# Kernel optimization log

Measured on AMD Instinct MI355X. Metric: run time of the kernel, lower is better.

## Reference

```python
import jax, jax.numpy as jnp
import numpy as np

NEG_SLOPE = 0.2  # PyG GATConv default negative_slope


def gat_conv(x, src, dst, n_nodes, W, a_src, a_dst, b, concat):
    # x: [N, F_in], W: [F_in, H*C], a_src/a_dst: [H, C], b: [H*C] or [C]
    H, C = a_src.shape
    h = (x @ W).reshape(n_nodes, H, C)              # [N, H, C]
    e_s = jnp.sum(h * a_src, axis=-1)               # [N, H]
    e_d = jnp.sum(h * a_dst, axis=-1)               # [N, H]
    e = jax.nn.leaky_relu(e_s[src] + e_d[dst], NEG_SLOPE)  # [E, H]
    # segment softmax over incoming edges of each destination node
    m = jax.ops.segment_max(e, dst, num_segments=n_nodes)
    m = jnp.where(jnp.isfinite(m), m, 0.0)
    p = jnp.exp(e - m[dst])                         # [E, H]
    s = jax.ops.segment_sum(p, dst, num_segments=n_nodes)
    alpha = p / (s[dst] + 1e-16)                    # [E, H]
    out = jax.ops.segment_sum(h[src] * alpha[:, :, None], dst, num_segments=n_nodes)  # [N, H, C]
    out = out.reshape(n_nodes, H * C) if concat else out.mean(axis=1)
    return out + b


def setup_inputs() -> dict:
    key = jax.random.key(0)
    ks = jax.random.split(key, 20)
    N, E = 50000, 800000
    F_in, C, H = 128, 64, 4
    sc = 0.05
    inp = {
        "x": jax.random.normal(ks[0], (N, F_in), dtype=jnp.float32),
        "edge_index": jax.random.randint(ks[1], (2, E), 0, N, dtype=jnp.int64),
        # conv1: F_in -> C x H heads, concat
        "W1": jax.random.normal(ks[2], (F_in, H * C), dtype=jnp.float32) * sc,
        "a1_src": jax.random.normal(ks[3], (H, C), dtype=jnp.float32) * sc,
        "a1_dst": jax.random.normal(ks[4], (H, C), dtype=jnp.float32) * sc,
        "b1": jnp.zeros((H * C,), dtype=jnp.float32),
        # conv2: H*C -> C x H heads, concat
        "W2": jax.random.normal(ks[5], (H * C, H * C), dtype=jnp.float32) * sc,
        "a2_src": jax.random.normal(ks[6], (H, C), dtype=jnp.float32) * sc,
        "a2_dst": jax.random.normal(ks[7], (H, C), dtype=jnp.float32) * sc,
        "b2": jnp.zeros((H * C,), dtype=jnp.float32),
        # conv3: H*C -> C, 1 head, concat=False (mean)
        "W3": jax.random.normal(ks[8], (H * C, C), dtype=jnp.float32) * sc,
        "a3_src": jax.random.normal(ks[9], (1, C), dtype=jnp.float32) * sc,
        "a3_dst": jax.random.normal(ks[10], (1, C), dtype=jnp.float32) * sc,
        "b3": jnp.zeros((C,), dtype=jnp.float32),
        # node classification head: C -> 2
        "cls_W": jax.random.normal(ks[11], (C, 2), dtype=jnp.float32) * sc,
        "cls_b": jnp.zeros((2,), dtype=jnp.float32),
    }
    return inp


def reference(x, edge_index, W1, a1_src, a1_dst, b1, W2, a2_src, a2_dst, b2,
              W3, a3_src, a3_dst, b3, cls_W, cls_b):
    N = x.shape[0]
    # PyG GATConv default: add self loops
    loop = jnp.arange(N, dtype=edge_index.dtype)
    ei = jnp.concatenate([edge_index, jnp.stack([loop, loop])], axis=1)
    src, dst = ei[0], ei[1]

    h = jax.nn.elu(gat_conv(x, src, dst, N, W1, a1_src, a1_dst, b1, concat=True))
    h = jax.nn.elu(gat_conv(h, src, dst, N, W2, a2_src, a2_dst, b2, concat=True))
    h = gat_conv(h, src, dst, N, W3, a3_src, a3_dst, b3, concat=False)  # [N, C]

    node_output = h @ cls_W + cls_b  # [N, 2]
    link_embedding = h               # [N, C]
    return node_output, link_embedding
```

## Files before the change

kernel.cpp:

```cpp
#include <hip/hip_runtime.h>
#include <math.h>


typedef unsigned short ushort;
typedef __attribute__((ext_vector_type(8))) short bf16x8;
typedef __attribute__((ext_vector_type(4))) float f32x4;

static __device__ __forceinline__ ushort f2bf(float f) {
    unsigned x = __float_as_uint(f);
    unsigned r = (x + 0x7FFF + ((x >> 16) & 1)) >> 16;
    return (ushort)r;
}
static __device__ __forceinline__ float bf2f(ushort u) {
    return __uint_as_float(((unsigned)u) << 16);
}


__global__ void count_deg(const int* __restrict__ ei, int E, int* __restrict__ deg) {
    int i = blockIdx.x * blockDim.x + threadIdx.x;
    int stride = gridDim.x * blockDim.x;
    for (int e = i; e < E; e += stride) {
        int d = ei[E + e];
        atomicAdd(&deg[d], 1);
    }
}

__global__ void scan_local(const int* __restrict__ deg, int* __restrict__ offsets,
                           int* __restrict__ blockSums, int N) {
    int tid = threadIdx.x;
    int lane = tid & 63;
    int wv = tid >> 6;
    int base = blockIdx.x * 1024 + tid * 4;
    int v[4];
#pragma unroll
    for (int j = 0; j < 4; ++j) {
        int idx = base + j;
        v[j] = (idx < N) ? (deg[idx] + 1) : 0;
    }
    int tsum = v[0] + v[1] + v[2] + v[3];
    int inc = tsum;
#pragma unroll
    for (int off = 1; off < 64; off <<= 1) {
        int u = __shfl_up(inc, off);
        if (lane >= off) inc += u;
    }
    __shared__ int wtot[4];
    if (lane == 63) wtot[wv] = inc;
    __syncthreads();
    int wbase = 0;
#pragma unroll
    for (int w = 0; w < 4; ++w)
        if (w < wv) wbase += wtot[w];
    int run = wbase + inc - tsum;
#pragma unroll
    for (int j = 0; j < 4; ++j) {
        int idx = base + j;
        if (idx < N) offsets[idx] = run;
        run += v[j];
    }
    if (tid == 255) blockSums[blockIdx.x] = wbase + inc;
}

__global__ void scan_blocks(const int* __restrict__ blockSums, int* __restrict__ blockBase,
                            int* __restrict__ offsets, int N, int nblk) {
    int lane = threadIdx.x & 63;
    int v = (lane < nblk) ? blockSums[lane] : 0;
    int inc = v;
#pragma unroll
    for (int off = 1; off < 64; off <<= 1) {
        int u = __shfl_up(inc, off);
        if (lane >= off) inc += u;
    }
    if (lane < nblk) blockBase[lane] = inc - v;
    if (lane == 63) offsets[N] = inc;
}

__global__ void scan_add(int* __restrict__ offsets, const int* __restrict__ blockBase, int N) {
    int i = blockIdx.x * blockDim.x + threadIdx.x;
    if (i < N) offsets[i] += blockBase[i >> 10];
}

__global__ void fill_self(const int* __restrict__ offsets, int* __restrict__ counter,
                          int* __restrict__ csr_src, int N) {
    int i = blockIdx.x * blockDim.x + threadIdx.x;
    if (i < N) {
        csr_src[offsets[i]] = i;
        counter[i] = 1;
    }
}

__global__ void fill_edges(const int* __restrict__ ei, int E,
                           const int* __restrict__ offsets, int* __restrict__ counter,
                           int* __restrict__ csr_src) {
    int i = blockIdx.x * blockDim.x + threadIdx.x;
    int stride = gridDim.x * blockDim.x;
    for (int e = i; e < E; e += stride) {
        int s = ei[e];
        int d = ei[E + e];
        int pos = offsets[d] + atomicAdd(&counter[d], 1);
        csr_src[pos] = s;
    }
}


__global__ void xsplit(const float* __restrict__ X, ushort* __restrict__ Xh,
                       ushort* __restrict__ Xl, int total4) {
    int i = blockIdx.x * blockDim.x + threadIdx.x;
    if (i >= total4) return;
    float4 v = *(const float4*)(X + (size_t)i * 4);
    ushort4 h, l;
    h.x = f2bf(v.x); l.x = f2bf(v.x - bf2f(h.x));
    h.y = f2bf(v.y); l.y = f2bf(v.y - bf2f(h.y));
    h.z = f2bf(v.z); l.z = f2bf(v.z - bf2f(h.z));
    h.w = f2bf(v.w); l.w = f2bf(v.w - bf2f(h.w));
    *(ushort4*)(Xh + (size_t)i * 4) = h;
    *(ushort4*)(Xl + (size_t)i * 4) = l;
}

__global__ void wsplit_t(const float* __restrict__ W, ushort* __restrict__ Wth,
                         ushort* __restrict__ Wtl, int K, int N) {
    int id = blockIdx.x * blockDim.x + threadIdx.x;
    if (id >= K * N) return;
    int k = id % K, n = id / K;
    float v = W[(size_t)k * N + n];
    ushort h = f2bf(v);
    Wth[id] = h;
    Wtl[id] = f2bf(v - bf2f(h));
}


template<int BN>
__global__ __launch_bounds__(256) void gemm_mfma(const ushort* __restrict__ Ah,
                                                 const ushort* __restrict__ Al,
                                                 const ushort* __restrict__ Bh,
                                                 const ushort* __restrict__ Bl,
                                                 float* __restrict__ Cmat,
                                                 int M, int N, int K) {
    constexpr int BK = 32, PAD = 8;
    constexpr int WAVES_N = BN / 64;
    constexpr int WAVES_M = 4 / WAVES_N;
    constexpr int WTM = 128 / WAVES_M;
    constexpr int MI = WTM / 16;
    constexpr int NI = 4;
    __shared__ ushort Atile[128][BK + PAD];
    __shared__ ushort Btile[BN][BK + PAD];

    int tid = threadIdx.x;
    int lane = tid & 63;
    int wid = tid >> 6;
    int fr = lane & 15;
    int fg = lane >> 4;
    int wm0 = (wid / WAVES_N) * WTM;
    int wn0 = (wid % WAVES_N) * 64;
    int mBase = blockIdx.x * 128;
    int nBase = blockIdx.y * BN;

    f32x4 acc[MI][NI];
#pragma unroll
    for (int mi = 0; mi < MI; ++mi)
#pragma unroll
        for (int ni = 0; ni < NI; ++ni) acc[mi][ni] = (f32x4)0.0f;

    const int KI = K / BK;
    for (int seg = 0; seg < 3; ++seg) {
        const ushort* Ap = (seg == 1) ? Al : Ah;
        const ushort* Bp = (seg == 2) ? Bl : Bh;
        for (int t = 0; t < KI; ++t) {
            int k0 = t * BK;
#pragma unroll
            for (int i = 0; i < 2; ++i) {
                int u = tid + i * 256;
                int row = u >> 2;
                int sl = (u & 3) * 8;
                int gm = mBase + row;
                if (gm >= M) gm = M - 1;
                bf16x8 v = *(const bf16x8*)(Ap + (size_t)gm * K + k0 + sl);
                *(bf16x8*)&Atile[row][sl] = v;
            }
#pragma unroll
            for (int i = 0; i < BN * BK / 8 / 256; ++i) {
                int u = tid + i * 256;
                int row = u >> 2;
                int sl = (u & 3) * 8;
                int gn = nBase + row;
                bf16x8 v = *(const bf16x8*)(Bp + (size_t)gn * K + k0 + sl);
                *(bf16x8*)&Btile[row][sl] = v;
            }
            __syncthreads();
            bf16x8 af[MI], bfr[NI];
#pragma unroll
            for (int mi = 0; mi < MI; ++mi)
                af[mi] = *(const bf16x8*)&Atile[wm0 + mi * 16 + fr][fg * 8];
#pragma unroll
            for (int ni = 0; ni < NI; ++ni)
                bfr[ni] = *(const bf16x8*)&Btile[wn0 + ni * 16 + fr][fg * 8];
#pragma unroll
            for (int mi = 0; mi < MI; ++mi)
#pragma unroll
                for (int ni = 0; ni < NI; ++ni)
                    acc[mi][ni] = __builtin_amdgcn_mfma_f32_16x16x32_bf16(
                        af[mi], bfr[ni], acc[mi][ni], 0, 0, 0);
            __syncthreads();
        }
    }

#pragma unroll
    for (int mi = 0; mi < MI; ++mi) {
#pragma unroll
        for (int j = 0; j < 4; ++j) {
            int gm = mBase + wm0 + mi * 16 + fg * 4 + j;
            if (gm >= M) continue;
#pragma unroll
            for (int ni = 0; ni < NI; ++ni) {
                int gn = nBase + wn0 + ni * 16 + fr;
                Cmat[(size_t)gm * N + gn] = acc[mi][ni][j];
            }
        }
    }
}


template<int HC, int H>
__global__ void attn_coef(const float* __restrict__ h,
                          const float* __restrict__ a_src,
                          const float* __restrict__ a_dst,
                          float* __restrict__ e_s, float* __restrict__ e_d,
                          ushort* __restrict__ hb, int N) {
    int wid = (int)((blockIdx.x * (size_t)blockDim.x + threadIdx.x) >> 6);
    int lane = threadIdx.x & 63;
    if (wid >= N) return;
    if constexpr (HC == 256) {
        float4 hv = *(const float4*)(h + (size_t)wid * 256 + lane * 4);
        float4 as = *(const float4*)(a_src + lane * 4);
        float4 ad = *(const float4*)(a_dst + lane * 4);
        ushort4 q;
        q.x = f2bf(hv.x); q.y = f2bf(hv.y); q.z = f2bf(hv.z); q.w = f2bf(hv.w);
        *(ushort4*)(hb + (size_t)wid * 256 + lane * 4) = q;
        float ps = hv.x * as.x + hv.y * as.y + hv.z * as.z + hv.w * as.w;
        float pd = hv.x * ad.x + hv.y * ad.y + hv.z * ad.z + hv.w * ad.w;
#pragma unroll
        for (int off = 1; off <= 8; off <<= 1) {
            ps += __shfl_xor(ps, off);
            pd += __shfl_xor(pd, off);
        }
        if ((lane & 15) == 0) {
            int hd = lane >> 4;
            e_s[(size_t)wid * H + hd] = ps;
            e_d[(size_t)wid * H + hd] = pd;
        }
    } else {
        float hv = h[(size_t)wid * HC + lane];
        hb[(size_t)wid * HC + lane] = f2bf(hv);
        float ps = hv * a_src[lane];
        float pd = hv * a_dst[lane];
#pragma unroll
        for (int off = 1; off <= 32; off <<= 1) {
            ps += __shfl_xor(ps, off);
            pd += __shfl_xor(pd, off);
        }
        if (lane == 0) {
            e_s[wid] = ps;
            e_d[wid] = pd;
        }
    }
}


template<int HC, int H, bool ELU, int U, bool SPLIT>
__global__ void aggregate(const ushort* __restrict__ hb,
                          const float* __restrict__ e_s, const float* __restrict__ e_d,
                          const int* __restrict__ offsets, const int* __restrict__ csr_src,
                          const float* __restrict__ bias,
                          float* __restrict__ out,
                          ushort* __restrict__ oh, ushort* __restrict__ ol, int N) {
    int wid = (int)((blockIdx.x * (size_t)blockDim.x + threadIdx.x) >> 6);
    int lane = threadIdx.x & 63;
    if (wid >= N) return;
    constexpr int VEC = HC / 64;
    constexpr int C = HC / H;
    int hd = (lane * VEC) / C;
    float ed = e_d[(size_t)wid * H + hd];
    int beg = offsets[wid], end = offsets[wid + 1];
    float m = -1e30f, s = 0.0f;
    float acc[VEC];
#pragma unroll
    for (int j = 0; j < VEC; ++j) acc[j] = 0.0f;

    for (int k = beg; k < end; k += U) {
        int sidx[U];
#pragma unroll
        for (int u = 0; u < U; ++u) {
            int kk = k + u;
            kk = (kk < end) ? kk : end - 1;
            sidx[u] = csr_src[kk];
        }
        float e[U];
#pragma unroll
        for (int u = 0; u < U; ++u) e[u] = e_s[(size_t)sidx[u] * H + hd];
        ushort4 hv4[U];
        ushort  hv1[U];
        if constexpr (VEC == 4) {
#pragma unroll
            for (int u = 0; u < U; ++u)
                hv4[u] = *(const ushort4*)(hb + (size_t)sidx[u] * HC + lane * 4);
        } else {
#pragma unroll
            for (int u = 0; u < U; ++u)
                hv1[u] = hb[(size_t)sidx[u] * HC + lane];
        }
#pragma unroll
        for (int u = 0; u < U; ++u) {
            float t = e[u] + ed;
            t = (t >= 0.0f) ? t : 0.2f * t;
            e[u] = (k + u < end) ? t : -1e30f;
        }
        float bm = -1e30f;
#pragma unroll
        for (int u = 0; u < U; ++u) bm = fmaxf(bm, e[u]);
        float nm = fmaxf(m, bm);
        float r = __expf(m - nm);
        float p[U];
        float psum = 0.0f;
#pragma unroll
        for (int u = 0; u < U; ++u) { p[u] = __expf(e[u] - nm); psum += p[u]; }
        s = s * r + psum;
        if constexpr (VEC == 4) {
#pragma unroll
            for (int j = 0; j < 4; ++j) acc[j] *= r;
#pragma unroll
            for (int u = 0; u < U; ++u) {
                acc[0] += p[u] * bf2f(hv4[u].x);
                acc[1] += p[u] * bf2f(hv4[u].y);
                acc[2] += p[u] * bf2f(hv4[u].z);
                acc[3] += p[u] * bf2f(hv4[u].w);
            }
        } else {
            acc[0] *= r;
#pragma unroll
            for (int u = 0; u < U; ++u) acc[0] += p[u] * bf2f(hv1[u]);
        }
        m = nm;
    }
    float inv = 1.0f / (s + 1e-16f);
    float o[VEC];
#pragma unroll
    for (int j = 0; j < VEC; ++j) {
        int f = lane * VEC + j;
        o[j] = acc[j] * inv + bias[f];
        if constexpr (ELU) o[j] = (o[j] > 0.0f) ? o[j] : expm1f(o[j]);
    }
    if constexpr (SPLIT) {
        if constexpr (VEC == 4) {
            ushort4 h4, l4;
            h4.x = f2bf(o[0]); l4.x = f2bf(o[0] - bf2f(h4.x));
            h4.y = f2bf(o[1]); l4.y = f2bf(o[1] - bf2f(h4.y));
            h4.z = f2bf(o[2]); l4.z = f2bf(o[2] - bf2f(h4.z));
            h4.w = f2bf(o[3]); l4.w = f2bf(o[3] - bf2f(h4.w));
            *(ushort4*)(oh + (size_t)wid * HC + lane * 4) = h4;
            *(ushort4*)(ol + (size_t)wid * HC + lane * 4) = l4;
        } else {
            ushort h1 = f2bf(o[0]);
            oh[(size_t)wid * HC + lane] = h1;
            ol[(size_t)wid * HC + lane] = f2bf(o[0] - bf2f(h1));
        }
    } else {
#pragma unroll
        for (int j = 0; j < VEC; ++j)
            out[(size_t)wid * HC + lane * VEC + j] = o[j];
    }
}


__global__ void cls_head(const float* __restrict__ h3, const float* __restrict__ W,
                         const float* __restrict__ b, float* __restrict__ out, int N) {
    int wid = (int)((blockIdx.x * (size_t)blockDim.x + threadIdx.x) >> 6);
    int lane = threadIdx.x & 63;
    if (wid >= N) return;
    float v = h3[(size_t)wid * 64 + lane];
    float p0 = v * W[lane * 2 + 0];
    float p1 = v * W[lane * 2 + 1];
#pragma unroll
    for (int off = 1; off <= 32; off <<= 1) {
        p0 += __shfl_xor(p0, off);
        p1 += __shfl_xor(p1, off);
    }
    if (lane == 0) {
        out[(size_t)wid * 2 + 0] = p0 + b[0];
        out[(size_t)wid * 2 + 1] = p1 + b[1];
    }
}


extern "C" void kernel_launch(void* const* d_in, const int* in_sizes, int n_in,
                              void* d_out, int out_size, void* d_ws, size_t ws_size,
                              hipStream_t stream) {
    const float* x      = (const float*)d_in[0];
    const int*   ei     = (const int*)d_in[1];
    const float* W1     = (const float*)d_in[2];
    const float* a1_src = (const float*)d_in[3];
    const float* a1_dst = (const float*)d_in[4];
    const float* b1     = (const float*)d_in[5];
    const float* W2     = (const float*)d_in[6];
    const float* a2_src = (const float*)d_in[7];
    const float* a2_dst = (const float*)d_in[8];
    const float* b2     = (const float*)d_in[9];
    const float* W3     = (const float*)d_in[10];
    const float* a3_src = (const float*)d_in[11];
    const float* a3_dst = (const float*)d_in[12];
    const float* b3     = (const float*)d_in[13];
    const float* cls_W  = (const float*)d_in[14];
    const float* cls_b  = (const float*)d_in[15];

    const int N = in_sizes[0] / 128;
    const int E = in_sizes[1] / 2;
    const int ET = E + N;
    const int HC = 256;
    const int nScanBlk = (N + 1023) / 1024;

    char* w = (char*)d_ws;
    auto carve = [&](size_t bytes) {
        char* p = w;
        w += (bytes + 255) & ~(size_t)255;
        return p;
    };
    int*    deg     = (int*)   carve((size_t)N * 4);
    int*    counter = (int*)   carve((size_t)N * 4);
    int*    offsets = (int*)   carve((size_t)(N + 1) * 4);
    int*    csr_src = (int*)   carve((size_t)ET * 4);
    int*    blkSums = (int*)   carve((size_t)64 * 4);
    int*    blkBase = (int*)   carve((size_t)64 * 4);
    float*  e_s     = (float*) carve((size_t)N * 4 * 4);
    float*  e_d     = (float*) carve((size_t)N * 4 * 4);
    float*  hbuf    = (float*) carve((size_t)N * HC * 4);
    ushort* hb      = (ushort*)carve((size_t)N * HC * 2);
    ushort* Ahi     = (ushort*)carve((size_t)N * HC * 2);
    ushort* Alo     = (ushort*)carve((size_t)N * HC * 2);
    ushort* W1th    = (ushort*)carve((size_t)128 * 256 * 2);
    ushort* W1tl    = (ushort*)carve((size_t)128 * 256 * 2);
    ushort* W2th    = (ushort*)carve((size_t)256 * 256 * 2);
    ushort* W2tl    = (ushort*)carve((size_t)256 * 256 * 2);
    ushort* W3th    = (ushort*)carve((size_t)256 * 64 * 2);
    ushort* W3tl    = (ushort*)carve((size_t)256 * 64 * 2);
    (void)ws_size;

    float* out_node = (float*)d_out;
    float* out_link = (float*)d_out + 2 * (size_t)N;

    hipMemsetAsync(deg, 0, (size_t)N * 4, stream);
    int eblocks = (E + 255) / 256;
    if (eblocks > 2048) eblocks = 2048;
    count_deg<<<eblocks, 256, 0, stream>>>(ei, E, deg);
    scan_local<<<nScanBlk, 256, 0, stream>>>(deg, offsets, blkSums, N);
    scan_blocks<<<1, 64, 0, stream>>>(blkSums, blkBase, offsets, N, nScanBlk);
    scan_add<<<(N + 255) / 256, 256, 0, stream>>>(offsets, blkBase, N);
    fill_self<<<(N + 255) / 256, 256, 0, stream>>>(offsets, counter, csr_src, N);
    fill_edges<<<eblocks, 256, 0, stream>>>(ei, E, offsets, counter, csr_src);

    xsplit<<<(N * 128 / 4 + 255) / 256, 256, 0, stream>>>(x, Ahi, Alo, N * 128 / 4);
    wsplit_t<<<(128 * 256 + 255) / 256, 256, 0, stream>>>(W1, W1th, W1tl, 128, 256);
    wsplit_t<<<(256 * 256 + 255) / 256, 256, 0, stream>>>(W2, W2th, W2tl, 256, 256);
    wsplit_t<<<(256 * 64 + 255) / 256, 256, 0, stream>>>(W3, W3th, W3tl, 256, 64);

    dim3 g12((N + 127) / 128, 2);
    dim3 g3((N + 127) / 128, 1);
    int nodeBlocks = (N + 3) / 4;

    gemm_mfma<128><<<g12, 256, 0, stream>>>(Ahi, Alo, W1th, W1tl, hbuf, N, 256, 128);
    attn_coef<256, 4><<<nodeBlocks, 256, 0, stream>>>(hbuf, a1_src, a1_dst, e_s, e_d, hb, N);
    aggregate<256, 4, true, 8, true><<<nodeBlocks, 256, 0, stream>>>(
        hb, e_s, e_d, offsets, csr_src, b1, nullptr, Ahi, Alo, N);
    gemm_mfma<128><<<g12, 256, 0, stream>>>(Ahi, Alo, W2th, W2tl, hbuf, N, 256, 256);
    attn_coef<256, 4><<<nodeBlocks, 256, 0, stream>>>(hbuf, a2_src, a2_dst, e_s, e_d, hb, N);
    aggregate<256, 4, true, 8, true><<<nodeBlocks, 256, 0, stream>>>(
        hb, e_s, e_d, offsets, csr_src, b2, nullptr, Ahi, Alo, N);
    gemm_mfma<64><<<g3, 256, 0, stream>>>(Ahi, Alo, W3th, W3tl, hbuf, N, 64, 256);
    attn_coef<64, 1><<<nodeBlocks, 256, 0, stream>>>(hbuf, a3_src, a3_dst, e_s, e_d, hb, N);
    aggregate<64, 1, false, 8, false><<<nodeBlocks, 256, 0, stream>>>(
        hb, e_s, e_d, offsets, csr_src, b3, out_link, nullptr, nullptr, N);
    cls_head<<<nodeBlocks, 256, 0, stream>>>(out_link, cls_W, cls_b, out_node, N);
}
```

Before: 428.3 us.

## Fuse split-bf16 GEMM passes, retile, and emit bf16 output directly

The GEMM now loads hi and lo tiles of A and B together and issues the three split-bf16 MFMAs per k-step in one loop, instead of three separate passes over K. Tiles change to 64 rows with the full N width per block, so each A row is read once. The GEMM writes bf16 output directly, and attn_coef reads that bf16 buffer, which removes the fp32 intermediate write and read. The attention coefficients are now computed from bf16-rounded h rather than fp32 h, a small precision loss, and shared memory per block doubles.

```diff
diff --git a/kernel.cpp b/kernel.cpp
--- a/kernel.cpp
+++ b/kernel.cpp
@@ -129,30 +129,27 @@
 }
 
 
-template<int BN>
+template<int BM, int BN, int WM, int WN>
 __global__ __launch_bounds__(256) void gemm_mfma(const ushort* __restrict__ Ah,
                                                  const ushort* __restrict__ Al,
                                                  const ushort* __restrict__ Bh,
                                                  const ushort* __restrict__ Bl,
-                                                 float* __restrict__ Cmat,
+                                                 ushort* __restrict__ Cb,
                                                  int M, int N, int K) {
     constexpr int BK = 32, PAD = 8;
-    constexpr int WAVES_N = BN / 64;
-    constexpr int WAVES_M = 4 / WAVES_N;
-    constexpr int WTM = 128 / WAVES_M;
-    constexpr int MI = WTM / 16;
-    constexpr int NI = 4;
-    __shared__ ushort Atile[128][BK + PAD];
-    __shared__ ushort Btile[BN][BK + PAD];
+    constexpr int MI = BM / WM / 16;
+    constexpr int NI = BN / WN / 16;
+    __shared__ ushort As[2][BM][BK + PAD];
+    __shared__ ushort Bs[2][BN][BK + PAD];
 
     int tid = threadIdx.x;
     int lane = tid & 63;
     int wid = tid >> 6;
     int fr = lane & 15;
     int fg = lane >> 4;
-    int wm0 = (wid / WAVES_N) * WTM;
-    int wn0 = (wid % WAVES_N) * 64;
-    int mBase = blockIdx.x * 128;
+    int wm0 = (wid / WN) * (BM / WM);
+    int wn0 = (wid % WN) * (BN / WN);
+    int mBase = blockIdx.x * BM;
     int nBase = blockIdx.y * BN;
 
     f32x4 acc[MI][NI];
@@ -161,47 +158,55 @@
 #pragma unroll
         for (int ni = 0; ni < NI; ++ni) acc[mi][ni] = (f32x4)0.0f;
 
+    constexpr int ACH = BM * BK / 8;
+    constexpr int BCH = BN * BK / 8;
+
     const int KI = K / BK;
-    for (int seg = 0; seg < 3; ++seg) {
-        const ushort* Ap = (seg == 1) ? Al : Ah;
-        const ushort* Bp = (seg == 2) ? Bl : Bh;
-        for (int t = 0; t < KI; ++t) {
-            int k0 = t * BK;
-#pragma unroll
-            for (int i = 0; i < 2; ++i) {
-                int u = tid + i * 256;
-                int row = u >> 2;
-                int sl = (u & 3) * 8;
-                int gm = mBase + row;
-                if (gm >= M) gm = M - 1;
-                bf16x8 v = *(const bf16x8*)(Ap + (size_t)gm * K + k0 + sl);
-                *(bf16x8*)&Atile[row][sl] = v;
+    for (int t = 0; t < KI; ++t) {
+        int k0 = t * BK;
+#pragma unroll
+        for (int q = tid; q < ACH; q += 256) {
+            int row = q >> 2;
+            int sl = (q & 3) * 8;
+            int gm = mBase + row;
+            if (gm >= M) gm = M - 1;
+            size_t off = (size_t)gm * K + k0 + sl;
+            *(bf16x8*)&As[0][row][sl] = *(const bf16x8*)(Ah + off);
+            *(bf16x8*)&As[1][row][sl] = *(const bf16x8*)(Al + off);
+        }
+#pragma unroll
+        for (int q = tid; q < BCH; q += 256) {
+            int row = q >> 2;
+            int sl = (q & 3) * 8;
+            size_t off = (size_t)(nBase + row) * K + k0 + sl;
+            *(bf16x8*)&Bs[0][row][sl] = *(const bf16x8*)(Bh + off);
+            *(bf16x8*)&Bs[1][row][sl] = *(const bf16x8*)(Bl + off);
+        }
+        __syncthreads();
+
+        bf16x8 afh[MI], afl[MI], bfh[NI], bfl[NI];
+#pragma unroll
+        for (int mi = 0; mi < MI; ++mi) {
+            afh[mi] = *(const bf16x8*)&As[0][wm0 + mi * 16 + fr][fg * 8];
+            afl[mi] = *(const bf16x8*)&As[1][wm0 + mi * 16 + fr][fg * 8];
+        }
+#pragma unroll
+        for (int ni = 0; ni < NI; ++ni) {
+            bfh[ni] = *(const bf16x8*)&Bs[0][wn0 + ni * 16 + fr][fg * 8];
+            bfl[ni] = *(const bf16x8*)&Bs[1][wn0 + ni * 16 + fr][fg * 8];
+        }
+#pragma unroll
+        for (int mi = 0; mi < MI; ++mi)
+#pragma unroll
+            for (int ni = 0; ni < NI; ++ni) {
+                acc[mi][ni] = __builtin_amdgcn_mfma_f32_16x16x32_bf16(
+                    afh[mi], bfh[ni], acc[mi][ni], 0, 0, 0);
+                acc[mi][ni] = __builtin_amdgcn_mfma_f32_16x16x32_bf16(
+                    afl[mi], bfh[ni], acc[mi][ni], 0, 0, 0);
+                acc[mi][ni] = __builtin_amdgcn_mfma_f32_16x16x32_bf16(
+                    afh[mi], bfl[ni], acc[mi][ni], 0, 0, 0);
             }
-#pragma unroll
-            for (int i = 0; i < BN * BK / 8 / 256; ++i) {
-                int u = tid + i * 256;
-                int row = u >> 2;
-                int sl = (u & 3) * 8;
-                int gn = nBase + row;
-                bf16x8 v = *(const bf16x8*)(Bp + (size_t)gn * K + k0 + sl);
-                *(bf16x8*)&Btile[row][sl] = v;
-            }
-            __syncthreads();
-            bf16x8 af[MI], bfr[NI];
-#pragma unroll
-            for (int mi = 0; mi < MI; ++mi)
-                af[mi] = *(const bf16x8*)&Atile[wm0 + mi * 16 + fr][fg * 8];
-#pragma unroll
-            for (int ni = 0; ni < NI; ++ni)
-                bfr[ni] = *(const bf16x8*)&Btile[wn0 + ni * 16 + fr][fg * 8];
-#pragma unroll
-            for (int mi = 0; mi < MI; ++mi)
-#pragma unroll
-                for (int ni = 0; ni < NI; ++ni)
-                    acc[mi][ni] = __builtin_amdgcn_mfma_f32_16x16x32_bf16(
-                        af[mi], bfr[ni], acc[mi][ni], 0, 0, 0);
-            __syncthreads();
-        }
+        __syncthreads();
     }
 
 #pragma unroll
@@ -213,7 +218,7 @@
 #pragma unroll
             for (int ni = 0; ni < NI; ++ni) {
                 int gn = nBase + wn0 + ni * 16 + fr;
-                Cmat[(size_t)gm * N + gn] = acc[mi][ni][j];
+                Cb[(size_t)gm * N + gn] = f2bf(acc[mi][ni][j]);
             }
         }
     }
@@ -221,23 +226,20 @@
 
 
 template<int HC, int H>
-__global__ void attn_coef(const float* __restrict__ h,
+__global__ void attn_coef(const ushort* __restrict__ hb,
                           const float* __restrict__ a_src,
                           const float* __restrict__ a_dst,
-                          float* __restrict__ e_s, float* __restrict__ e_d,
-                          ushort* __restrict__ hb, int N) {
+                          float* __restrict__ e_s, float* __restrict__ e_d, int N) {
     int wid = (int)((blockIdx.x * (size_t)blockDim.x + threadIdx.x) >> 6);
     int lane = threadIdx.x & 63;
     if (wid >= N) return;
     if constexpr (HC == 256) {
-        float4 hv = *(const float4*)(h + (size_t)wid * 256 + lane * 4);
+        ushort4 q = *(const ushort4*)(hb + (size_t)wid * 256 + lane * 4);
         float4 as = *(const float4*)(a_src + lane * 4);
         float4 ad = *(const float4*)(a_dst + lane * 4);
-        ushort4 q;
-        q.x = f2bf(hv.x); q.y = f2bf(hv.y); q.z = f2bf(hv.z); q.w = f2bf(hv.w);
-        *(ushort4*)(hb + (size_t)wid * 256 + lane * 4) = q;
-        float ps = hv.x * as.x + hv.y * as.y + hv.z * as.z + hv.w * as.w;
-        float pd = hv.x * ad.x + hv.y * ad.y + hv.z * ad.z + hv.w * ad.w;
+        float h0 = bf2f(q.x), h1 = bf2f(q.y), h2 = bf2f(q.z), h3 = bf2f(q.w);
+        float ps = h0 * as.x + h1 * as.y + h2 * as.z + h3 * as.w;
+        float pd = h0 * ad.x + h1 * ad.y + h2 * ad.z + h3 * ad.w;
 #pragma unroll
         for (int off = 1; off <= 8; off <<= 1) {
             ps += __shfl_xor(ps, off);
@@ -249,8 +251,7 @@
             e_d[(size_t)wid * H + hd] = pd;
         }
     } else {
-        float hv = h[(size_t)wid * HC + lane];
-        hb[(size_t)wid * HC + lane] = f2bf(hv);
+        float hv = bf2f(hb[(size_t)wid * HC + lane]);
         float ps = hv * a_src[lane];
         float pd = hv * a_dst[lane];
 #pragma unroll
@@ -431,7 +432,6 @@
     int*    blkBase = (int*)   carve((size_t)64 * 4);
     float*  e_s     = (float*) carve((size_t)N * 4 * 4);
     float*  e_d     = (float*) carve((size_t)N * 4 * 4);
-    float*  hbuf    = (float*) carve((size_t)N * HC * 4);
     ushort* hb      = (ushort*)carve((size_t)N * HC * 2);
     ushort* Ahi     = (ushort*)carve((size_t)N * HC * 2);
     ushort* Alo     = (ushort*)carve((size_t)N * HC * 2);
@@ -461,20 +461,20 @@
     wsplit_t<<<(256 * 256 + 255) / 256, 256, 0, stream>>>(W2, W2th, W2tl, 256, 256);
     wsplit_t<<<(256 * 64 + 255) / 256, 256, 0, stream>>>(W3, W3th, W3tl, 256, 64);
 
-    dim3 g12((N + 127) / 128, 2);
-    dim3 g3((N + 127) / 128, 1);
+    dim3 g12((N + 63) / 64, 1);
+    dim3 g3((N + 63) / 64, 1);
     int nodeBlocks = (N + 3) / 4;
 
-    gemm_mfma<128><<<g12, 256, 0, stream>>>(Ahi, Alo, W1th, W1tl, hbuf, N, 256, 128);
-    attn_coef<256, 4><<<nodeBlocks, 256, 0, stream>>>(hbuf, a1_src, a1_dst, e_s, e_d, hb, N);
+    gemm_mfma<64, 256, 1, 4><<<g12, 256, 0, stream>>>(Ahi, Alo, W1th, W1tl, hb, N, 256, 128);
+    attn_coef<256, 4><<<nodeBlocks, 256, 0, stream>>>(hb, a1_src, a1_dst, e_s, e_d, N);
     aggregate<256, 4, true, 8, true><<<nodeBlocks, 256, 0, stream>>>(
         hb, e_s, e_d, offsets, csr_src, b1, nullptr, Ahi, Alo, N);
-    gemm_mfma<128><<<g12, 256, 0, stream>>>(Ahi, Alo, W2th, W2tl, hbuf, N, 256, 256);
-    attn_coef<256, 4><<<nodeBlocks, 256, 0, stream>>>(hbuf, a2_src, a2_dst, e_s, e_d, hb, N);
+    gemm_mfma<64, 256, 1, 4><<<g12, 256, 0, stream>>>(Ahi, Alo, W2th, W2tl, hb, N, 256, 256);
+    attn_coef<256, 4><<<nodeBlocks, 256, 0, stream>>>(hb, a2_src, a2_dst, e_s, e_d, N);
     aggregate<256, 4, true, 8, true><<<nodeBlocks, 256, 0, stream>>>(
         hb, e_s, e_d, offsets, csr_src, b2, nullptr, Ahi, Alo, N);
-    gemm_mfma<64><<<g3, 256, 0, stream>>>(Ahi, Alo, W3th, W3tl, hbuf, N, 64, 256);
-    attn_coef<64, 1><<<nodeBlocks, 256, 0, stream>>>(hbuf, a3_src, a3_dst, e_s, e_d, hb, N);
+    gemm_mfma<64, 64, 2, 2><<<g3, 256, 0, stream>>>(Ahi, Alo, W3th, W3tl, hb, N, 64, 256);
+    attn_coef<64, 1><<<nodeBlocks, 256, 0, stream>>>(hb, a3_src, a3_dst, e_s, e_d, N);
     aggregate<64, 1, false, 8, false><<<nodeBlocks, 256, 0, stream>>>(
         hb, e_s, e_d, offsets, csr_src, b3, out_link, nullptr, nullptr, N);
     cls_head<<<nodeBlocks, 256, 0, stream>>>(out_link, cls_W, cls_b, out_node, N);
```

Measured after the change: 402.1 us. -6.1%, faster.
